# Optimization experiments

Hardware: AMD Instinct MI355X
Metric: run time of the kernel (lower is better)

The kernel has to match this reference:

```python
import jax, jax.numpy as jnp
import numpy as np

B = 1024      # batch
D = 512       # input/output dim per module
H = 1024      # expert hidden dim
T = 8         # num_tasks
NTE = 2       # experts per task
NSE = 2       # shared experts
E = T * NTE + NSE   # 18 experts per layer
# expert_input_idx: each expert reads the module it belongs to (tasks 0..7, shared=8)
EXPERT_IDX = np.array([m for m in range(T + 1) for _ in range(2)])  # [E]


def _lin_init(k, shape, fan_in):
    s = 1.0 / np.sqrt(fan_in)
    return jax.random.uniform(k, shape, jnp.float32, -s, s)


def setup_inputs() -> dict:
    key = jax.random.key(0)
    ks = jax.random.split(key, 20)
    inp = {"inputs": jax.random.normal(ks[0], (B, T + 1, D), jnp.float32)}
    # layer 0: experts D->H->D (stacked over E), gates for M=9 modules
    inp["W1_0"] = _lin_init(ks[1], (E, D, H), D)
    inp["b1_0"] = _lin_init(ks[2], (E, H), D)
    inp["W2_0"] = _lin_init(ks[3], (E, H, D), H)
    inp["b2_0"] = _lin_init(ks[4], (E, D), H)
    inp["Wg_0"] = _lin_init(ks[5], (T + 1, D, E), D)
    inp["bg_0"] = _lin_init(ks[6], (T + 1, E), D)
    # layer 1 (final): gates only for M=T modules
    inp["W1_1"] = _lin_init(ks[7], (E, D, H), D)
    inp["b1_1"] = _lin_init(ks[8], (E, H), D)
    inp["W2_1"] = _lin_init(ks[9], (E, H, D), H)
    inp["b2_1"] = _lin_init(ks[10], (E, D), H)
    inp["Wg_1"] = _lin_init(ks[11], (T, D, E), D)
    inp["bg_1"] = _lin_init(ks[12], (T, E), D)
    # self-exp residual weights: per task [L=2, NTE], shared [L-1=1, NSE]
    sc = 1.0 / np.sqrt(NTE)
    inp["sew_task"] = jax.random.uniform(ks[13], (T, 2, NTE), jnp.float32, -sc, sc)
    inp["sew_shared"] = jax.random.uniform(ks[14], (1, NSE), jnp.float32, -sc, sc)
    return inp


def _build_add(rows):
    # rows: list of [2]-vectors, one per fully-active module; block-diagonal layout
    M = len(rows)
    add = jnp.zeros((M, E), jnp.float32)
    for m, w in enumerate(rows):
        add = add.at[m, 2 * m:2 * m + 2].set(w)
    return add


def _layer(x, W1, b1, W2, b2, Wg, bg, add):
    # x: [B, M_in, D]; experts share input of their owning module
    xe = x[:, EXPERT_IDX, :]                                   # [B, E, D]
    h = jax.nn.relu(jnp.einsum('bed,edh->beh', xe, W1) + b1)   # [B, E, H]
    eo = jnp.einsum('beh,eho->beo', h, W2) + b2                # [B, E, D]
    M = Wg.shape[0]
    g = jax.nn.softmax(jnp.einsum('bmd,mde->bme', x[:, :M, :], Wg) + bg, axis=-1)
    g = g + add[None]                                          # self-exp residual
    return jnp.einsum('bme,beo->bmo', g, eo)                   # [B, M, D]


def reference(inputs, W1_0, b1_0, W2_0, b2_0, Wg_0, bg_0,
              W1_1, b1_1, W2_1, b2_1, Wg_1, bg_1, sew_task, sew_shared):
    add0 = _build_add([sew_task[t, 0] for t in range(T)] + [sew_shared[0]])  # [T+1, E]
    add1 = _build_add([sew_task[t, 1] for t in range(T)])                    # [T, E]
    x = _layer(inputs, W1_0, b1_0, W2_0, b2_0, Wg_0, bg_0, add0)  # [B, T+1, D]
    x = _layer(x, W1_1, b1_1, W2_1, b2_1, Wg_1, bg_1, add1)       # [B, T, D]
    return x
```

## Files before the change

### kernel.cpp

```cpp
#include <hip/hip_runtime.h>

typedef unsigned short u16;
typedef unsigned int u32;
typedef __attribute__((ext_vector_type(8))) short short8;
typedef __attribute__((ext_vector_type(4))) float floatx4;

#define GLOAD_LDS16(gp, lp)                                                              \
  __builtin_amdgcn_global_load_lds((const __attribute__((address_space(1))) void*)(gp),  \
                                   (__attribute__((address_space(3))) void*)(lp), 16, 0, 0)

__device__ __forceinline__ u16 f2bf(float f) {
  u32 u = __float_as_uint(f);
  u += 0x7fffu + ((u >> 16) & 1u);
  return (u16)(u >> 16);
}

__device__ __forceinline__ void bf8_to_f(const u16* p, float* o) {
  const uint4 v = *(const uint4*)p;
  const u32 a[4] = {v.x, v.y, v.z, v.w};
#pragma unroll
  for (int i = 0; i < 4; i++) {
    o[2 * i]     = __uint_as_float(a[i] << 16);
    o[2 * i + 1] = __uint_as_float(a[i] & 0xffff0000u);
  }
}

__global__ __launch_bounds__(256) void prep_w_kernel(
    const float* __restrict__ W1a, const float* __restrict__ W2a,
    const float* __restrict__ W1b, const float* __restrict__ W2b,
    u16* __restrict__ T1a, u16* __restrict__ T2a,
    u16* __restrict__ T1b, u16* __restrict__ T2b) {
  __shared__ float tile[64][65];
  const int id = blockIdx.x;
  const int t = threadIdx.x;

  const int tsel = id / 2304;
  const int rem = id % 2304;
  const int e = rem >> 7;
  const int t128 = rem & 127;
  const int K = (tsel & 1) ? 1024 : 512;
  const int N = (tsel & 1) ? 512 : 1024;
  const int kt = (tsel & 1) ? (t128 & 15) : (t128 & 7);
  const int nt = (tsel & 1) ? (t128 >> 4) : (t128 >> 3);
  const int k0 = kt * 64, n0 = nt * 64;
  const float* W = (tsel == 0) ? W1a : (tsel == 1) ? W2a : (tsel == 2) ? W1b : W2b;
  u16* WT = (tsel == 0) ? T1a : (tsel == 1) ? T2a : (tsel == 2) ? T1b : T2b;

  const float* Wp = W + ((size_t)e * K + k0) * N + n0;
  const int r = t >> 4;
  const int c = (t & 15) << 2;
#pragma unroll
  for (int p = 0; p < 4; p++) {
    const int row = r + p * 16;
    const float4 v = *(const float4*)(Wp + (size_t)row * N + c);
    tile[row][c + 0] = v.x; tile[row][c + 1] = v.y;
    tile[row][c + 2] = v.z; tile[row][c + 3] = v.w;
  }
  __syncthreads();
  u16* WTp = WT + ((size_t)e * N + n0) * K + k0;
#pragma unroll
  for (int p = 0; p < 4; p++) {
    const int row = r + p * 16;
    u32 lo = (u32)f2bf(tile[c + 0][row]) | ((u32)f2bf(tile[c + 1][row]) << 16);
    u32 hi = (u32)f2bf(tile[c + 2][row]) | ((u32)f2bf(tile[c + 3][row]) << 16);
    *(uint2*)(WTp + (size_t)row * K + c) = make_uint2(lo, hi);
  }
}

__global__ __launch_bounds__(256) void prep_misc_kernel(
    const float* __restrict__ Wg0, const float* __restrict__ Wg1,
    u16* __restrict__ WgT0, u16* __restrict__ WgT1,
    const float* __restrict__ x0, u16* __restrict__ x0bf) {
  const int id = blockIdx.x;
  const int t = threadIdx.x;
  if (id < 612) {
    int idx = id * 256 + t;
    const float* Wg = Wg0;
    u16* WgT = WgT0;
    if (idx >= 82944) { idx -= 82944; Wg = Wg1; WgT = WgT1; }
    const int d = idx & 511;
    const int r = idx >> 9;
    const int e = r % 18;
    const int m = r / 18;
    WgT[idx] = f2bf(Wg[((size_t)(m * 512 + d)) * 18 + e]);
  } else {
    const int i = (id - 612) * 256 + t;
    const float4 v = ((const float4*)x0)[i];
    u32 lo = (u32)f2bf(v.x) | ((u32)f2bf(v.y) << 16);
    u32 hi = (u32)f2bf(v.z) | ((u32)f2bf(v.w) << 16);
    ((uint2*)x0bf)[i] = make_uint2(lo, hi);
  }
}

template <int M, int LAYER>
__device__ __forceinline__ void gating_body(
    int bid, const u16* __restrict__ xbf, const u16* __restrict__ WgT,
    const float* __restrict__ bg, const float* __restrict__ sew_task,
    const float* __restrict__ sew_shared, float* __restrict__ wsm) {
  const int lane = threadIdx.x & 63;
  const int wave = threadIdx.x >> 6;
  const int m = bid >> 7;
  const int b0 = (bid & 127) * 8 + wave * 2;

  float xa[8], xb[8];
  bf8_to_f(xbf + (size_t)b0 * 4608 + m * 512 + lane * 8, xa);
  bf8_to_f(xbf + (size_t)(b0 + 1) * 4608 + m * 512 + lane * 8, xb);

  float lg0[18], lg1[18];
#pragma unroll
  for (int e = 0; e < 18; e++) {
    float w[8];
    bf8_to_f(WgT + ((size_t)m * 18 + e) * 512 + lane * 8, w);
    float s0 = 0.f, s1 = 0.f;
#pragma unroll
    for (int i = 0; i < 8; i++) { s0 = fmaf(w[i], xa[i], s0); s1 = fmaf(w[i], xb[i], s1); }
#pragma unroll
    for (int off = 1; off < 64; off <<= 1) {
      s0 += __shfl_xor(s0, off, 64);
      s1 += __shfl_xor(s1, off, 64);
    }
    const float bgv = bg[m * 18 + e];
    lg0[e] = s0 + bgv;
    lg1[e] = s1 + bgv;
  }
  float mx0 = lg0[0], mx1 = lg1[0];
#pragma unroll
  for (int e = 1; e < 18; e++) { mx0 = fmaxf(mx0, lg0[e]); mx1 = fmaxf(mx1, lg1[e]); }
  float sum0 = 0.f, sum1 = 0.f;
#pragma unroll
  for (int e = 0; e < 18; e++) { sum0 += __expf(lg0[e] - mx0); sum1 += __expf(lg1[e] - mx1); }
  float my0 = lg0[0], my1 = lg1[0];
#pragma unroll
  for (int e = 1; e < 18; e++)
    if (lane == e) { my0 = lg0[e]; my1 = lg1[e]; }
  float w0 = __expf(my0 - mx0) / sum0;
  float w1 = __expf(my1 - mx1) / sum1;
  if ((lane >> 1) == m) {
    float add;
    if (M == 9 && m == 8) add = sew_shared[lane & 1];
    else                  add = sew_task[m * 4 + 2 * LAYER + (lane & 1)];
    w0 += add; w1 += add;
  }
  if (lane < 18) {
    wsm[((size_t)b0 * M + m) * 18 + lane] = w0;
    wsm[((size_t)(b0 + 1) * M + m) * 18 + lane] = w1;
  }
}

template <bool RELU_BF16_OUT, int M, int LAYER, bool GATE>
__global__ __launch_bounds__(256, 3) void gemm_fused_kernel(
    const u16* __restrict__ A, const u16* __restrict__ BT,
    const float* __restrict__ bias, void* __restrict__ Cout,
    int lda, int a_shift, int a_mul, int ldc, int c_mul, int N, int K, int nshift, int G,
    const u16* __restrict__ WgT, const float* __restrict__ bg,
    const float* __restrict__ sewt, const float* __restrict__ sews,
    float* __restrict__ wsm) {
  if (GATE && (int)blockIdx.x >= G) {
    gating_body<M, LAYER>(blockIdx.x - G, A, WgT, bg, sewt, sews, wsm);
    return;
  }
  __shared__ __align__(16) u16 As[128 * 64];
  __shared__ __align__(16) u16 Bs[128 * 64];

  const int tid = threadIdx.x;
  const int lane = tid & 63;
  const int wave = tid >> 6;

  const int L = blockIdx.x;
  const int per_xcd = G >> 3;
  const int g = (L & 7) * per_xcd + (L >> 3);
  const int e = g >> nshift;
  const int wb = g & ((1 << nshift) - 1);
  const int mt = wb & 7;
  const int nt = wb >> 3;
  const int m0 = mt << 7, n0 = nt << 7;

  const u16* Aexp = A + (size_t)((e >> a_shift) * a_mul);
  const u16* Bexp = BT + (size_t)e * (size_t)N * (size_t)K;

  const int colsw = (((lane & 7) ^ ((lane >> 3) & 7)) << 3);
  const u16* aptr[4];
  const u16* bptr[4];
  u16* lA[4];
  u16* lB[4];
#pragma unroll
  for (int i = 0; i < 4; i++) {
    const int cch = wave * 4 + i;
    const int row = cch * 8 + (lane >> 3);
    aptr[i] = Aexp + (size_t)(m0 + row) * lda + colsw;
    bptr[i] = Bexp + (size_t)(n0 + row) * K + colsw;
    lA[i] = As + cch * 512;
    lB[i] = Bs + cch * 512;
  }

  floatx4 acc[4][4];
#pragma unroll
  for (int i = 0; i < 4; i++)
#pragma unroll
    for (int j = 0; j < 4; j++) acc[i][j] = (floatx4){0.f, 0.f, 0.f, 0.f};

  const int wm = (wave & 1) << 6;
  const int wn = (wave >> 1) << 6;
  const int r15 = lane & 15;
  const int quad = lane >> 4;

  int aoff[4], boff[4];
#pragma unroll
  for (int i = 0; i < 4; i++) {
    const int ra = wm + i * 16 + r15;
    aoff[i] = ra * 64 + ((quad ^ (ra & 7)) << 3);
    const int rb = wn + i * 16 + r15;
    boff[i] = rb * 64 + ((quad ^ (rb & 7)) << 3);
  }

  for (int k0 = 0; k0 < K; k0 += 64) {
    __syncthreads();
#pragma unroll
    for (int i = 0; i < 4; i++) GLOAD_LDS16(aptr[i] + k0, lA[i]);
#pragma unroll
    for (int i = 0; i < 4; i++) GLOAD_LDS16(bptr[i] + k0, lB[i]);
    __syncthreads();
#pragma unroll
    for (int s = 0; s < 2; s++) {
      short8 af[4], bfr[4];
#pragma unroll
      for (int i = 0; i < 4; i++) af[i] = *(const short8*)(As + (aoff[i] ^ (s << 5)));
#pragma unroll
      for (int j = 0; j < 4; j++) bfr[j] = *(const short8*)(Bs + (boff[j] ^ (s << 5)));
      __builtin_amdgcn_s_setprio(1);
#pragma unroll
      for (int i = 0; i < 4; i++)
#pragma unroll
        for (int j = 0; j < 4; j++)
          acc[i][j] = __builtin_amdgcn_mfma_f32_16x16x32_bf16(af[i], bfr[j], acc[i][j], 0, 0, 0);
      __builtin_amdgcn_s_setprio(0);
    }
  }

  const int ccol0 = n0 + wn + r15;
  const int crow0 = m0 + wm + quad * 4;
  float bv[4];
#pragma unroll
  for (int j = 0; j < 4; j++) bv[j] = bias[e * N + ccol0 + j * 16];

  if constexpr (RELU_BF16_OUT) {
    u16* Co = (u16*)Cout + (size_t)e * c_mul;
#pragma unroll
    for (int i = 0; i < 4; i++)
#pragma unroll
      for (int r = 0; r < 4; r++) {
        const size_t rowoff = (size_t)(crow0 + i * 16 + r) * ldc;
#pragma unroll
        for (int j = 0; j < 4; j++) {
          float v = acc[i][j][r] + bv[j];
          v = v > 0.f ? v : 0.f;
          Co[rowoff + ccol0 + j * 16] = f2bf(v);
        }
      }
  } else {
    float* Co = (float*)Cout + (size_t)e * c_mul;
#pragma unroll
    for (int i = 0; i < 4; i++)
#pragma unroll
      for (int r = 0; r < 4; r++) {
        const size_t rowoff = (size_t)(crow0 + i * 16 + r) * ldc;
#pragma unroll
        for (int j = 0; j < 4; j++) Co[rowoff + ccol0 + j * 16] = acc[i][j][r] + bv[j];
      }
  }
}

template <int M, bool BF16OUT>
__global__ __launch_bounds__(256) void wsum_kernel(
    const float* __restrict__ eo, const float* __restrict__ wsm,
    float* __restrict__ outf, u16* __restrict__ outb) {
  __shared__ float ws[2 * M * 18];
  const int t = threadIdx.x;
  const int b0 = blockIdx.x * 2;
  for (int i = t; i < 2 * M * 18; i += 256) ws[i] = wsm[(size_t)b0 * M * 18 + i];
  __syncthreads();
  const int lb = t >> 7;
  const int s = t & 127;
  const int b = b0 + lb;
  const float* eob = eo + (size_t)b * 9216 + s * 4;
  const float* wr = ws + lb * M * 18;

  float4 acc[M];
#pragma unroll
  for (int m = 0; m < M; m++) acc[m] = make_float4(0.f, 0.f, 0.f, 0.f);
#pragma unroll
  for (int e = 0; e < 18; e++) {
    const float4 v = *(const float4*)(eob + e * 512);
#pragma unroll
    for (int m = 0; m < M; m++) {
      const float w = wr[m * 18 + e];
      acc[m].x = fmaf(w, v.x, acc[m].x);
      acc[m].y = fmaf(w, v.y, acc[m].y);
      acc[m].z = fmaf(w, v.z, acc[m].z);
      acc[m].w = fmaf(w, v.w, acc[m].w);
    }
  }
  if constexpr (BF16OUT) {
    u16* ob = outb + (size_t)b * 4608 + s * 4;
#pragma unroll
    for (int m = 0; m < M; m++) {
      u32 lo = (u32)f2bf(acc[m].x) | ((u32)f2bf(acc[m].y) << 16);
      u32 hi = (u32)f2bf(acc[m].z) | ((u32)f2bf(acc[m].w) << 16);
      *(uint2*)(ob + m * 512) = make_uint2(lo, hi);
    }
  } else {
    float* ob = outf + (size_t)b * (M * 512) + s * 4;
#pragma unroll
    for (int m = 0; m < M; m++) *(float4*)(ob + m * 512) = acc[m];
  }
}

extern "C" void kernel_launch(void* const* d_in, const int* in_sizes, int n_in,
                              void* d_out, int out_size, void* d_ws, size_t ws_size,
                              hipStream_t stream) {
  const float* x0   = (const float*)d_in[0];
  const float* W1_0 = (const float*)d_in[1];
  const float* b1_0 = (const float*)d_in[2];
  const float* W2_0 = (const float*)d_in[3];
  const float* b2_0 = (const float*)d_in[4];
  const float* Wg_0 = (const float*)d_in[5];
  const float* bg_0 = (const float*)d_in[6];
  const float* W1_1 = (const float*)d_in[7];
  const float* b1_1 = (const float*)d_in[8];
  const float* W2_1 = (const float*)d_in[9];
  const float* b2_1 = (const float*)d_in[10];
  const float* Wg_1 = (const float*)d_in[11];
  const float* bg_1 = (const float*)d_in[12];
  const float* sewt = (const float*)d_in[13];
  const float* sews = (const float*)d_in[14];
  float* out = (float*)d_out;

  char* p = (char*)d_ws;
  auto take = [&](size_t n) { char* r = p; p += (n + 255) & ~(size_t)255; return r; };
  u16*   x0bf = (u16*)take(4718592ull * 2);
  u16*   W1T0 = (u16*)take(9437184ull * 2);
  u16*   W2T0 = (u16*)take(9437184ull * 2);
  u16*   W1T1 = (u16*)take(9437184ull * 2);
  u16*   W2T1 = (u16*)take(9437184ull * 2);
  u16*   WgT0 = (u16*)take(82944ull * 2);
  u16*   WgT1 = (u16*)take(73728ull * 2);
  u16*   hbf  = (u16*)take(18874368ull * 2);
  float* eo   = (float*)take(9437184ull * 4);
  u16*   x1bf = (u16*)take(4718592ull * 2);
  float* wsm0 = (float*)take(165888ull * 4);
  float* wsm1 = (float*)take(147456ull * 4);

  dim3 blk(256);
  prep_w_kernel<<<dim3(9216), blk, 0, stream>>>(W1_0, W2_0, W1_1, W2_1,
                                                W1T0, W2T0, W1T1, W2T1);
  prep_misc_kernel<<<dim3(5220), blk, 0, stream>>>(Wg_0, Wg_1, WgT0, WgT1, x0, x0bf);
  gemm_fused_kernel<true, 9, 0, true><<<dim3(1152 + 1152), blk, 0, stream>>>(
      x0bf, W1T0, b1_0, (void*)hbf, 4608, 1, 512, 18432, 1024, 1024, 512, 6, 1152,
      WgT0, bg_0, sewt, sews, wsm0);
  gemm_fused_kernel<false, 9, 0, false><<<dim3(576), blk, 0, stream>>>(
      hbf, W2T0, b2_0, (void*)eo, 18432, 0, 1024, 9216, 512, 512, 1024, 5, 576,
      nullptr, nullptr, nullptr, nullptr, nullptr);
  wsum_kernel<9, true><<<dim3(512), blk, 0, stream>>>(eo, wsm0, nullptr, x1bf);
  gemm_fused_kernel<true, 8, 1, true><<<dim3(1152 + 1024), blk, 0, stream>>>(
      x1bf, W1T1, b1_1, (void*)hbf, 4608, 1, 512, 18432, 1024, 1024, 512, 6, 1152,
      WgT1, bg_1, sewt, sews, wsm1);
  gemm_fused_kernel<false, 8, 1, false><<<dim3(576), blk, 0, stream>>>(
      hbf, W2T1, b2_1, (void*)eo, 18432, 0, 1024, 9216, 512, 512, 1024, 5, 576,
      nullptr, nullptr, nullptr, nullptr, nullptr);
  wsum_kernel<8, false><<<dim3(512), blk, 0, stream>>>(eo, wsm1, out, nullptr);
}
```

Before: 371.5 us.

## Overlap weight transposes with preceding GEMM launches by appending transpose blocks

The single up-front prep kernel that converted and transposed all four expert weight tensors is split up. Only W1 of layer 0 is transposed before the first GEMM. The other three transposes are appended as extra blocks to the GEMM launch that runs just before each tensor is first needed, so conversion overlaps with compute and the GPU stays fuller. Shared memory is unified into one buffer reused by the GEMM tiles and the transpose tile. This adds control-flow branching and grid imbalance to the GEMM kernels, and the transpose blocks compete with GEMM blocks for bandwidth.

Result: faster. 335.7 us (-9.6%).

```diff
diff --git a/kernel.cpp b/kernel.cpp
--- a/kernel.cpp
+++ b/kernel.cpp
@@ -25,26 +25,17 @@
   }
 }
 
-__global__ __launch_bounds__(256) void prep_w_kernel(
-    const float* __restrict__ W1a, const float* __restrict__ W2a,
-    const float* __restrict__ W1b, const float* __restrict__ W2b,
-    u16* __restrict__ T1a, u16* __restrict__ T2a,
-    u16* __restrict__ T1b, u16* __restrict__ T2b) {
-  __shared__ float tile[64][65];
-  const int id = blockIdx.x;
+__device__ __forceinline__ void transpose_body(int id, const float* __restrict__ W,
+                                               u16* __restrict__ WT, int mode,
+                                               float* tile ) {
   const int t = threadIdx.x;
-
-  const int tsel = id / 2304;
-  const int rem = id % 2304;
-  const int e = rem >> 7;
-  const int t128 = rem & 127;
-  const int K = (tsel & 1) ? 1024 : 512;
-  const int N = (tsel & 1) ? 512 : 1024;
-  const int kt = (tsel & 1) ? (t128 & 15) : (t128 & 7);
-  const int nt = (tsel & 1) ? (t128 >> 4) : (t128 >> 3);
+  const int e = id >> 7;
+  const int t128 = id & 127;
+  const int K = mode ? 1024 : 512;
+  const int N = mode ? 512 : 1024;
+  const int kt = mode ? (t128 & 15) : (t128 & 7);
+  const int nt = mode ? (t128 >> 4) : (t128 >> 3);
   const int k0 = kt * 64, n0 = nt * 64;
-  const float* W = (tsel == 0) ? W1a : (tsel == 1) ? W2a : (tsel == 2) ? W1b : W2b;
-  u16* WT = (tsel == 0) ? T1a : (tsel == 1) ? T2a : (tsel == 2) ? T1b : T2b;
 
   const float* Wp = W + ((size_t)e * K + k0) * N + n0;
   const int r = t >> 4;
@@ -53,28 +44,32 @@
   for (int p = 0; p < 4; p++) {
     const int row = r + p * 16;
     const float4 v = *(const float4*)(Wp + (size_t)row * N + c);
-    tile[row][c + 0] = v.x; tile[row][c + 1] = v.y;
-    tile[row][c + 2] = v.z; tile[row][c + 3] = v.w;
+    tile[row * 65 + c + 0] = v.x; tile[row * 65 + c + 1] = v.y;
+    tile[row * 65 + c + 2] = v.z; tile[row * 65 + c + 3] = v.w;
   }
   __syncthreads();
   u16* WTp = WT + ((size_t)e * N + n0) * K + k0;
 #pragma unroll
   for (int p = 0; p < 4; p++) {
     const int row = r + p * 16;
-    u32 lo = (u32)f2bf(tile[c + 0][row]) | ((u32)f2bf(tile[c + 1][row]) << 16);
-    u32 hi = (u32)f2bf(tile[c + 2][row]) | ((u32)f2bf(tile[c + 3][row]) << 16);
+    u32 lo = (u32)f2bf(tile[(c + 0) * 65 + row]) | ((u32)f2bf(tile[(c + 1) * 65 + row]) << 16);
+    u32 hi = (u32)f2bf(tile[(c + 2) * 65 + row]) | ((u32)f2bf(tile[(c + 3) * 65 + row]) << 16);
     *(uint2*)(WTp + (size_t)row * K + c) = make_uint2(lo, hi);
   }
 }
 
-__global__ __launch_bounds__(256) void prep_misc_kernel(
+__global__ __launch_bounds__(256) void prep1_kernel(
+    const float* __restrict__ W1a, u16* __restrict__ T1a,
     const float* __restrict__ Wg0, const float* __restrict__ Wg1,
     u16* __restrict__ WgT0, u16* __restrict__ WgT1,
     const float* __restrict__ x0, u16* __restrict__ x0bf) {
+  __shared__ float tile[64 * 65];
   const int id = blockIdx.x;
   const int t = threadIdx.x;
-  if (id < 612) {
-    int idx = id * 256 + t;
+  if (id < 2304) {
+    transpose_body(id, W1a, T1a, 0, tile);
+  } else if (id < 2916) {
+    int idx = (id - 2304) * 256 + t;
     const float* Wg = Wg0;
     u16* WgT = WgT0;
     if (idx >= 82944) { idx -= 82944; Wg = Wg1; WgT = WgT1; }
@@ -84,7 +79,7 @@
     const int m = r / 18;
     WgT[idx] = f2bf(Wg[((size_t)(m * 512 + d)) * 18 + e]);
   } else {
-    const int i = (id - 612) * 256 + t;
+    const int i = (id - 2916) * 256 + t;
     const float4 v = ((const float4*)x0)[i];
     u32 lo = (u32)f2bf(v.x) | ((u32)f2bf(v.y) << 16);
     u32 hi = (u32)f2bf(v.z) | ((u32)f2bf(v.w) << 16);
@@ -147,20 +142,27 @@
   }
 }
 
-template <bool RELU_BF16_OUT, int M, int LAYER, bool GATE>
+template <bool RELU_BF16_OUT, int M, int LAYER, bool GATE, bool TRANS>
 __global__ __launch_bounds__(256, 3) void gemm_fused_kernel(
     const u16* __restrict__ A, const u16* __restrict__ BT,
     const float* __restrict__ bias, void* __restrict__ Cout,
     int lda, int a_shift, int a_mul, int ldc, int c_mul, int N, int K, int nshift, int G,
     const u16* __restrict__ WgT, const float* __restrict__ bg,
     const float* __restrict__ sewt, const float* __restrict__ sews,
-    float* __restrict__ wsm) {
-  if (GATE && (int)blockIdx.x >= G) {
-    gating_body<M, LAYER>(blockIdx.x - G, A, WgT, bg, sewt, sews, wsm);
+    float* __restrict__ wsm,
+    int gate_cnt, const float* __restrict__ Wsrc, u16* __restrict__ Wdst, int wmode) {
+  __shared__ __align__(16) u16 smem[16384];
+  if ((GATE || TRANS) && (int)blockIdx.x >= G) {
+    const int rr = blockIdx.x - G;
+    if (GATE && rr < gate_cnt) {
+      gating_body<M, LAYER>(rr, A, WgT, bg, sewt, sews, wsm);
+      return;
+    }
+    if (TRANS) transpose_body(rr - (GATE ? gate_cnt : 0), Wsrc, Wdst, wmode, (float*)smem);
     return;
   }
-  __shared__ __align__(16) u16 As[128 * 64];
-  __shared__ __align__(16) u16 Bs[128 * 64];
+  u16* As = smem;
+  u16* Bs = smem + 8192;
 
   const int tid = threadIdx.x;
   const int lane = tid & 63;
@@ -351,21 +353,20 @@
   float* wsm1 = (float*)take(147456ull * 4);
 
   dim3 blk(256);
-  prep_w_kernel<<<dim3(9216), blk, 0, stream>>>(W1_0, W2_0, W1_1, W2_1,
-                                                W1T0, W2T0, W1T1, W2T1);
-  prep_misc_kernel<<<dim3(5220), blk, 0, stream>>>(Wg_0, Wg_1, WgT0, WgT1, x0, x0bf);
-  gemm_fused_kernel<true, 9, 0, true><<<dim3(1152 + 1152), blk, 0, stream>>>(
+  prep1_kernel<<<dim3(7524), blk, 0, stream>>>(W1_0, W1T0, Wg_0, Wg_1, WgT0, WgT1,
+                                               x0, x0bf);
+  gemm_fused_kernel<true, 9, 0, true, true><<<dim3(1152 + 1152 + 2304), blk, 0, stream>>>(
       x0bf, W1T0, b1_0, (void*)hbf, 4608, 1, 512, 18432, 1024, 1024, 512, 6, 1152,
-      WgT0, bg_0, sewt, sews, wsm0);
-  gemm_fused_kernel<false, 9, 0, false><<<dim3(576), blk, 0, stream>>>(
+      WgT0, bg_0, sewt, sews, wsm0, 1152, W2_0, W2T0, 1);
+  gemm_fused_kernel<false, 9, 0, false, true><<<dim3(576 + 2304), blk, 0, stream>>>(
       hbf, W2T0, b2_0, (void*)eo, 18432, 0, 1024, 9216, 512, 512, 1024, 5, 576,
-      nullptr, nullptr, nullptr, nullptr, nullptr);
+      nullptr, nullptr, nullptr, nullptr, nullptr, 0, W1_1, W1T1, 0);
   wsum_kernel<9, true><<<dim3(512), blk, 0, stream>>>(eo, wsm0, nullptr, x1bf);
-  gemm_fused_kernel<true, 8, 1, true><<<dim3(1152 + 1024), blk, 0, stream>>>(
+  gemm_fused_kernel<true, 8, 1, true, true><<<dim3(1152 + 1024 + 2304), blk, 0, stream>>>(
       x1bf, W1T1, b1_1, (void*)hbf, 4608, 1, 512, 18432, 1024, 1024, 512, 6, 1152,
-      WgT1, bg_1, sewt, sews, wsm1);
-  gemm_fused_kernel<false, 8, 1, false><<<dim3(576), blk, 0, stream>>>(
+      WgT1, bg_1, sewt, sews, wsm1, 1024, W2_1, W2T1, 1);
+  gemm_fused_kernel<false, 8, 1, false, false><<<dim3(576), blk, 0, stream>>>(
       hbf, W2T1, b2_1, (void*)eo, 18432, 0, 1024, 9216, 512, 512, 1024, 5, 576,
-      nullptr, nullptr, nullptr, nullptr, nullptr);
+      nullptr, nullptr, nullptr, nullptr, nullptr, 0, nullptr, nullptr, 0);
   wsum_kernel<8, false><<<dim3(512), blk, 0, stream>>>(eo, wsm1, out, nullptr);
 }
```
